# Kernel optimization log

Hardware: AMD Instinct MI355X
Metric: run time of the kernel (lower is better)

The kernel has to match this reference:

```python
import jax, jax.numpy as jnp
import numpy as np

N, E, IN_DIM, HID = 50000, 800000, 128, 64
NEG_SLOPE = 0.01  # torch F.leaky_relu default


def setup_inputs() -> dict:
    key = jax.random.key(0)
    ks = jax.random.split(key, 8)
    x = jax.random.normal(ks[0], (N, IN_DIM), jnp.float32)
    edge_index = jax.random.randint(ks[1], (2, E), 0, N, dtype=jnp.int32)
    edge_weight = jax.random.uniform(ks[2], (E,), jnp.float32)
    h = jnp.zeros((N, HID), jnp.float32)
    c = jnp.zeros((N, HID), jnp.float32)
    sx = 1.0 / np.sqrt(IN_DIM)
    sh = 1.0 / np.sqrt(HID)
    # gate order along leading axis: [i, f, c(tilde), o]; K=2 Chebyshev weights
    Wx = (jax.random.normal(ks[3], (4, 2, IN_DIM, HID), jnp.float32) * sx)
    bx = jnp.zeros((4, HID), jnp.float32)
    Wh = (jax.random.normal(ks[4], (4, 2, HID, HID), jnp.float32) * sh)
    bh = jnp.zeros((4, HID), jnp.float32)
    wc = jax.random.normal(ks[5], (3, HID), jnp.float32) * 0.1  # peepholes for i, f, o
    bg = jnp.zeros((4, HID), jnp.float32)
    W_head = jax.random.normal(ks[6], (HID, 1), jnp.float32) * sh
    b_head = jnp.zeros((1,), jnp.float32)
    return dict(x=x, edge_index=edge_index, edge_weight=edge_weight, h=h, c=c,
                Wx=Wx, bx=bx, Wh=Wh, bh=bh, wc=wc, bg=bg, W_head=W_head, b_head=b_head)


def _cheb_norm(src, dst, ew, n):
    # ChebConv 'sym' normalization with lambda_max=2: L_hat = -D^{-1/2} A D^{-1/2}
    # (the +1 self-loop from the Laplacian cancels against fill_value=-1)
    deg = jnp.zeros((n,), ew.dtype).at[src].add(ew)
    dinv = jnp.where(deg > 0, 1.0 / jnp.sqrt(jnp.where(deg > 0, deg, 1.0)), 0.0)
    return -dinv[src] * ew * dinv[dst]


def _prop(feat, src, dst, norm, n):
    # T1 = L_hat @ feat via edge gather + segment-sum
    return jax.ops.segment_sum(norm[:, None] * feat[src], dst, num_segments=n)


def reference(x, edge_index, edge_weight, h, c, Wx, bx, Wh, bh, wc, bg, W_head, b_head):
    n = x.shape[0]
    src, dst = edge_index[0], edge_index[1]
    norm = _cheb_norm(src, dst, edge_weight, n)
    Tx = _prop(x, src, dst, norm, n)
    Th = _prop(h, src, dst, norm, n)  # shared across all 4 h-side ChebConvs
    # z[g] = X W[g,0] + (L_hat X) W[g,1] + b  for all gates at once
    z = (jnp.einsum('nd,gdh->gnh', x, Wx[:, 0]) + jnp.einsum('nd,gdh->gnh', Tx, Wx[:, 1]) + bx[:, None, :]
         + jnp.einsum('nd,gdh->gnh', h, Wh[:, 0]) + jnp.einsum('nd,gdh->gnh', Th, Wh[:, 1]) + bh[:, None, :])
    i = jax.nn.sigmoid(z[0] + wc[0] * c + bg[0])
    f = jax.nn.sigmoid(z[1] + wc[1] * c + bg[1])
    g = jnp.tanh(z[2] + bg[2])
    c_new = f * c + i * g
    o = jax.nn.sigmoid(z[3] + wc[2] * c_new + bg[3])
    h_new = o * jnp.tanh(c_new)
    out = jax.nn.leaky_relu(h_new, NEG_SLOPE) @ W_head + b_head
    return out, h_new, c_new
```

## Files before the change

kernel.cpp:

```cpp
#include <hip/hip_runtime.h>
#include <hip/hip_bf16.h>

#define IN_DIM 128
#define HID 64
#define NEG_SLOPE 0.01f
#define CAP 5120

typedef __attribute__((ext_vector_type(8))) short short8;
typedef __attribute__((ext_vector_type(4))) short short4v;
typedef __attribute__((ext_vector_type(4))) float f32x4;
typedef unsigned short ushort_t;
typedef unsigned int uint_t;

__device__ __forceinline__ float fsig(float x) { return 1.f / (1.f + __expf(-x)); }
__device__ __forceinline__ float ftanh(float x) { return 1.f - 2.f / (__expf(2.f * x) + 1.f); }

__device__ __forceinline__ ushort_t f2bf(float f) {
    uint_t u = __float_as_uint(f);
    uint_t r = u + 0x7fffu + ((u >> 16) & 1u);
    return (ushort_t)(r >> 16);
}
__device__ __forceinline__ float bf2f(ushort_t s) { return __uint_as_float(((uint_t)s) << 16); }
__device__ __forceinline__ float bf2f_s(short s) { return bf2f((ushort_t)s); }

__global__ __launch_bounds__(256) void part_kernel(
    const int* __restrict__ src, const int* __restrict__ dst, const float* __restrict__ ew,
    const float* __restrict__ x, const float* __restrict__ h,
    const float* __restrict__ Wx, const float* __restrict__ Wh,
    int* __restrict__ cur_d, int* __restrict__ cur_s,
    int2* __restrict__ dpart, int2* __restrict__ spart,
    uint_t* __restrict__ xb_u, uint_t* __restrict__ hb_u, ushort_t* __restrict__ Wp,
    int E, int N, int nbPart) {
    __shared__ int hd[256], hs[256];
    int t = threadIdx.x;

    if (blockIdx.x < nbPart) {
        hd[t] = 0; hs[t] = 0;
        __syncthreads();
        int base = blockIdx.x * 2048;
        int sv[8], dv[8]; float wv[8];
#pragma unroll
        for (int it = 0; it < 8; ++it) {
            int e = base + it * 256 + t;
            bool ok = e < E;
            sv[it] = ok ? src[e] : 0;
            dv[it] = ok ? dst[e] : 0;
            wv[it] = ok ? ew[e] : 0.f;
            if (ok) {
                atomicAdd(&hd[dv[it] >> 8], 1);
                atomicAdd(&hs[sv[it] >> 8], 1);
            }
        }
        __syncthreads();
        int nd = hd[t], ns = hs[t];
        __syncthreads();
        if (nd) hd[t] = atomicAdd(&cur_d[t * 16], nd);
        if (ns) hs[t] = atomicAdd(&cur_s[t * 16], ns);
        __syncthreads();
#pragma unroll
        for (int it = 0; it < 8; ++it) {
            int e = base + it * 256 + t;
            if (e < E) {
                int d = dv[it], s = sv[it];
                int bd = d >> 8, bs = s >> 8;
                int pd = atomicAdd(&hd[bd], 1);
                int ps = atomicAdd(&hs[bs], 1);
                dpart[(size_t)bd * CAP + pd] = make_int2(s | ((d & 255) << 16), __float_as_int(wv[it]));
                spart[(size_t)bs * CAP + ps] = make_int2(s & 255, __float_as_int(wv[it]));
            }
        }
    }

    int tid = blockIdx.x * 256 + t;
    int T = gridDim.x * 256;
    int ncvt = N * 96;
    int nx = N * 64;
    for (int i = tid; i < ncvt; i += T) {
        if (i < nx) {
            float2 v = ((const float2*)x)[i];
            xb_u[i] = (uint_t)f2bf(v.x) | ((uint_t)f2bf(v.y) << 16);
        } else {
            int j = i - nx;
            float2 v = ((const float2*)h)[j];
            hb_u[j] = (uint_t)f2bf(v.x) | ((uint_t)f2bf(v.y) << 16);
        }
    }

    for (int idx = tid; idx < 384 * 256; idx += T) {
        int j = idx & 7;
        int tmp = idx >> 3;
        int lane = tmp & 63;
        int t2 = tmp >> 6;
        int ct = t2 & 15;
        int ks = t2 >> 4;
        int k = ks * 32 + (lane >> 4) * 8 + j;
        int colg = ct * 16 + (lane & 15);
        int g = colg >> 6, hdd = colg & 63;
        float v;
        if (k < 128)      v = Wx[((g * 2 + 0) * 128 + k) * 64 + hdd];
        else if (k < 192) v = Wh[((g * 2 + 0) * 64 + (k - 128)) * 64 + hdd];
        else if (k < 320) v = Wx[((g * 2 + 1) * 128 + (k - 192)) * 64 + hdd];
        else              v = Wh[((g * 2 + 1) * 64 + (k - 320)) * 64 + hdd];
        Wp[idx] = f2bf(v);
    }
}

__global__ __launch_bounds__(256) void deg_kernel(const int2* __restrict__ spart,
                                                  const int* __restrict__ cur_s,
                                                  float* __restrict__ dinv, int N) {
    __shared__ float df[256];
    int t = threadIdx.x, b = blockIdx.x;
    df[t] = 0.f;
    __syncthreads();
    int cnt = cur_s[b * 16];
    for (int i = t; i < cnt; i += 256) {
        int2 r = spart[(size_t)b * CAP + i];
        atomicAdd(&df[r.x & 255], __int_as_float(r.y));
    }
    __syncthreads();
    int g = b * 256 + t;
    if (g < N) {
        float dd = df[t];
        dinv[g] = dd > 0.f ? rsqrtf(dd) : 0.f;
    }
}

__global__ __launch_bounds__(256) void fillb_kernel(const int2* __restrict__ dpart,
                                                    const int* __restrict__ cur_d,
                                                    const float* __restrict__ dinv,
                                                    int* __restrict__ rowptr, int* __restrict__ rowend,
                                                    int2* __restrict__ eprm, int N) {
    __shared__ int c[256], sdata[256], pcur[256];
    __shared__ float dl[256];
    int t = threadIdx.x, b = blockIdx.x;
    c[t] = 0;
    int g = b * 256 + t;
    dl[t] = (g < N) ? dinv[g] : 0.f;
    __syncthreads();
    int cnt = cur_d[b * 16];
    for (int i = t; i < cnt; i += 256) {
        int m = dpart[(size_t)b * CAP + i].x;
        atomicAdd(&c[(m >> 16) & 255], 1);
    }
    __syncthreads();
    sdata[t] = c[t];
    __syncthreads();
    for (int off = 1; off < 256; off <<= 1) {
        int tmp = (t >= off) ? sdata[t - off] : 0;
        __syncthreads();
        sdata[t] += tmp;
        __syncthreads();
    }
    int excl = sdata[t] - c[t];
    pcur[t] = excl;
    if (g < N) {
        rowptr[g] = b * CAP + excl;
        rowend[g] = b * CAP + sdata[t];
    }
    __syncthreads();
    for (int i = t; i < cnt; i += 256) {
        int2 r = dpart[(size_t)b * CAP + i];
        int m = r.x;
        int dlo = (m >> 16) & 255;
        int s = m & 0xffff;
        float w = __int_as_float(r.y);
        int pos = atomicAdd(&pcur[dlo], 1);
        float nrm = -dinv[s] * w * dl[dlo];
        eprm[(size_t)b * CAP + pos] = make_int2(s, __float_as_int(nrm));
    }
}

#define GQ_LOAD(SS, WW, XV, HV, QOFF)                                          \
    _Pragma("unroll")                                                          \
    for (int q = 0; q < 4; ++q) {                                              \
        SS[q] = __shfl(sv, sl0 + (QOFF) + q);                                  \
        WW[q] = __shfl(wv, sl0 + (QOFF) + q);                                  \
        XV[q] = *(const short8*)(xb + (size_t)SS[q] * 128 + l16 * 8);          \
        HV[q] = *(const short4v*)(hb + (size_t)SS[q] * 64 + l16 * 4);          \
    }

#define GQ_FMA(WW, XV, HV)                                                     \
    _Pragma("unroll")                                                          \
    for (int q = 0; q < 4; ++q) {                                              \
        _Pragma("unroll")                                                      \
        for (int i = 0; i < 8; ++i) ax[i] += WW[q] * bf2f_s(XV[q][i]);         \
        _Pragma("unroll")                                                      \
        for (int i = 0; i < 4; ++i) ah[i] += WW[q] * bf2f_s(HV[q][i]);         \
    }

__global__ __launch_bounds__(256) void gather_kernel(const int* __restrict__ rowptr,
                                                     const int* __restrict__ rowend,
                                                     const int2* __restrict__ eprm,
                                                     const ushort_t* __restrict__ xb,
                                                     const ushort_t* __restrict__ hb,
                                                     ushort_t* __restrict__ Txb,
                                                     ushort_t* __restrict__ Thb, int N) {
    int lane = threadIdx.x & 63;
    int wave = threadIdx.x >> 6;
    int grp = lane >> 4, l16 = lane & 15;
    int node = blockIdx.x * 16 + wave * 4 + grp;
    bool valid = node < N;
    int p = 0, end = 0;
    if (valid) { p = rowptr[node]; end = rowend[node]; }

    float ax[8] = {0.f, 0.f, 0.f, 0.f, 0.f, 0.f, 0.f, 0.f};
    float ah[4] = {0.f, 0.f, 0.f, 0.f};

    int idx0 = p + l16;
    int2 pr = (idx0 < end) ? eprm[idx0] : make_int2(0, 0);

    int sl0 = grp * 16;
    for (int base = p; base < end; base += 16) {
        int2 cur = pr;
        int nidx = base + 16 + l16;
        if (base + 16 < end) pr = (nidx < end) ? eprm[nidx] : make_int2(0, 0);
        int sv = cur.x;
        float wv = __int_as_float(cur.y);

        int sA[4]; float wA[4]; short8 xA[4]; short4v hA[4];
        int sB[4]; float wB[4]; short8 xB[4]; short4v hB[4];
        GQ_LOAD(sA, wA, xA, hA, 0)
        GQ_LOAD(sB, wB, xB, hB, 4)
        GQ_FMA(wA, xA, hA)
        GQ_LOAD(sA, wA, xA, hA, 8)
        GQ_FMA(wB, xB, hB)
        GQ_LOAD(sB, wB, xB, hB, 12)
        GQ_FMA(wA, xA, hA)
        GQ_FMA(wB, xB, hB)
    }

    if (valid) {
        short8 tx;
#pragma unroll
        for (int i = 0; i < 8; ++i) tx[i] = (short)f2bf(ax[i]);
        *(short8*)(Txb + (size_t)node * 128 + l16 * 8) = tx;
        short4v th;
#pragma unroll
        for (int i = 0; i < 4; ++i) th[i] = (short)f2bf(ah[i]);
        *(short4v*)(Thb + (size_t)node * 64 + l16 * 4) = th;
    }
}

__global__ __launch_bounds__(256, 4) void fused_mfma(
    const ushort_t* __restrict__ xb, const ushort_t* __restrict__ hb,
    const ushort_t* __restrict__ Txb, const ushort_t* __restrict__ Thb,
    const float* __restrict__ c_in, const ushort_t* __restrict__ Wp,
    const float* __restrict__ bx, const float* __restrict__ bh,
    const float* __restrict__ wc, const float* __restrict__ bg,
    const float* __restrict__ Whead, const float* __restrict__ bhead,
    float* __restrict__ out, int N) {
    __shared__ ushort_t Bs[2][8192];
    int tid = threadIdx.x;
    int lane = tid & 63;
    int wave = tid >> 6;
    int quad = lane >> 4, m = lane & 15;
    int row0 = (blockIdx.x * 4 + wave) * 16;
    int ar = row0 + m; if (ar >= N) ar = N - 1;
    int ko = quad * 8;

    short8 afr[12];
#pragma unroll
    for (int ks = 0; ks < 12; ++ks) {
        const ushort_t* a;
        if (ks < 4)       a = xb  + (size_t)ar * 128 + ks * 32 + ko;
        else if (ks < 6)  a = hb  + (size_t)ar * 64 + (ks - 4) * 32 + ko;
        else if (ks < 10) a = Txb + (size_t)ar * 128 + (ks - 6) * 32 + ko;
        else              a = Thb + (size_t)ar * 64 + (ks - 10) * 32 + ko;
        afr[ks] = *(const short8*)a;
    }

    {
        const float4* gsrc = (const float4*)(Wp);
        float4* ldst = (float4*)Bs[0];
#pragma unroll
        for (int i = 0; i < 4; ++i) ldst[tid + 256 * i] = gsrc[tid + 256 * i];
    }

    f32x4 acc[16];
#pragma unroll
    for (int ct = 0; ct < 16; ++ct) {
        int g = ct >> 2, hd = (ct & 3) * 16 + m;
        float b = bx[g * 64 + hd] + bh[g * 64 + hd];
        f32x4 bb = {b, b, b, b};
        acc[ct] = bb;
    }

    __syncthreads();

#pragma unroll
    for (int ks = 0; ks < 12; ++ks) {
        int buf = ks & 1;
        float4 tmp[4];
        if (ks < 11) {
            const float4* gsrc = (const float4*)(Wp + (ks + 1) * 8192);
#pragma unroll
            for (int i = 0; i < 4; ++i) tmp[i] = gsrc[tid + 256 * i];
        }
        const short8* bsp = (const short8*)Bs[buf];
#pragma unroll
        for (int ct = 0; ct < 16; ++ct) {
            short8 bf = bsp[ct * 64 + lane];
            acc[ct] = __builtin_amdgcn_mfma_f32_16x16x32_bf16(afr[ks], bf, acc[ct], 0, 0, 0);
        }
        if (ks < 11) {
            float4* ldst = (float4*)Bs[buf ^ 1];
#pragma unroll
            for (int i = 0; i < 4; ++i) ldst[tid + 256 * i] = tmp[i];
            __syncthreads();
        }
    }

    float hp[4] = {0.f, 0.f, 0.f, 0.f};
    float bhv = bhead[0];

#pragma unroll
    for (int hs = 0; hs < 4; ++hs) {
        int hd = hs * 16 + m;
        float wc0 = wc[hd], wc1 = wc[64 + hd], wc2 = wc[128 + hd];
        float bg0 = bg[hd], bg1 = bg[64 + hd], bg2 = bg[128 + hd], bg3 = bg[192 + hd];
        float wh = Whead[hd];
#pragma unroll
        for (int reg = 0; reg < 4; ++reg) {
            int n = row0 + quad * 4 + reg;
            if (n < N) {
                float c_old = c_in[(size_t)n * 64 + hd];
                float zi = acc[0 * 4 + hs][reg];
                float zf = acc[1 * 4 + hs][reg];
                float zg = acc[2 * 4 + hs][reg];
                float zo = acc[3 * 4 + hs][reg];
                float ii = fsig(zi + wc0 * c_old + bg0);
                float ff = fsig(zf + wc1 * c_old + bg1);
                float gg = ftanh(zg + bg2);
                float cn = ff * c_old + ii * gg;
                float oo = fsig(zo + wc2 * cn + bg3);
                float hn = oo * ftanh(cn);
                out[N + (size_t)n * 64 + hd] = hn;
                out[N + (size_t)N * 64 + (size_t)n * 64 + hd] = cn;
                float lr = hn > 0.f ? hn : NEG_SLOPE * hn;
                hp[reg] += lr * wh;
            }
        }
    }
#pragma unroll
    for (int reg = 0; reg < 4; ++reg) {
        float v0 = hp[reg];
#pragma unroll
        for (int mask = 1; mask < 16; mask <<= 1) v0 += __shfl_xor(v0, mask);
        if (m == 0) {
            int n0_ = row0 + quad * 4 + reg;
            if (n0_ < N) out[n0_] = v0 + bhv;
        }
    }
}

extern "C" void kernel_launch(void* const* d_in, const int* in_sizes, int n_in,
                              void* d_out, int out_size, void* d_ws, size_t ws_size,
                              hipStream_t stream) {
    const float* x = (const float*)d_in[0];
    const int* ei = (const int*)d_in[1];
    const float* ew = (const float*)d_in[2];
    const float* h = (const float*)d_in[3];
    const float* c = (const float*)d_in[4];
    const float* Wx = (const float*)d_in[5];
    const float* bx = (const float*)d_in[6];
    const float* Wh = (const float*)d_in[7];
    const float* bh = (const float*)d_in[8];
    const float* wc = (const float*)d_in[9];
    const float* bg = (const float*)d_in[10];
    const float* Whead = (const float*)d_in[11];
    const float* bhead = (const float*)d_in[12];

    int N = in_sizes[0] / IN_DIM;
    int E = in_sizes[1] / 2;
    const int* src = ei;
    const int* dst = ei + E;

    int nbuck = (N + 255) >> 8;
    int nbPart = (E + 2047) / 2048;

    char* wp = (char*)d_ws;
    auto alloc = [&](size_t bytes) {
        char* p = wp;
        wp += (bytes + 255) & ~(size_t)255;
        return p;
    };
    int* cur = (int*)alloc((size_t)2 * nbuck * 16 * 4);
    int* cur_d = cur;
    int* cur_s = cur + (size_t)nbuck * 16;
    float* dinv = (float*)alloc((size_t)N * 4);
    int* rowptr = (int*)alloc((size_t)N * 4);
    int* rowend = (int*)alloc((size_t)N * 4);
    int2* dpart = (int2*)alloc((size_t)nbuck * CAP * 8);
    int2* spart = (int2*)alloc((size_t)nbuck * CAP * 8);
    int2* eprm = spart;
    ushort_t* xb = (ushort_t*)alloc((size_t)N * 128 * 2);
    ushort_t* hb = (ushort_t*)alloc((size_t)N * 64 * 2);
    ushort_t* Txb = (ushort_t*)alloc((size_t)N * 128 * 2);
    ushort_t* Thb = (ushort_t*)alloc((size_t)N * 64 * 2);
    ushort_t* Wp = (ushort_t*)alloc((size_t)384 * 256 * 2);

    hipMemsetAsync(cur, 0, (size_t)2 * nbuck * 16 * 4, stream);

    part_kernel<<<1024, 256, 0, stream>>>(src, dst, ew, x, h, Wx, Wh,
                                          cur_d, cur_s, dpart, spart,
                                          (uint_t*)xb, (uint_t*)hb, Wp, E, N, nbPart);
    deg_kernel<<<nbuck, 256, 0, stream>>>(spart, cur_s, dinv, N);
    fillb_kernel<<<nbuck, 256, 0, stream>>>(dpart, cur_d, dinv, rowptr, rowend, eprm, N);
    gather_kernel<<<(N + 15) / 16, 256, 0, stream>>>(rowptr, rowend, eprm, xb, hb, Txb, Thb, N);
    fused_mfma<<<(N + 63) / 64, 256, 0, stream>>>(xb, hb, Txb, Thb, c, Wp, bx, bh, wc, bg,
                                                  Whead, bhead, (float*)d_out, N);
}
```

Measured before the change: 253.8 us.

## Fuse gather into MFMA kernel and merge degree and fill passes

```diff
diff --git a/kernel.cpp b/kernel.cpp
--- a/kernel.cpp
+++ b/kernel.cpp
@@ -105,68 +105,63 @@
     }
 }
 
-__global__ __launch_bounds__(256) void deg_kernel(const int2* __restrict__ spart,
-                                                  const int* __restrict__ cur_s,
-                                                  float* __restrict__ dinv, int N) {
-    __shared__ float df[256];
-    int t = threadIdx.x, b = blockIdx.x;
-    df[t] = 0.f;
-    __syncthreads();
-    int cnt = cur_s[b * 16];
-    for (int i = t; i < cnt; i += 256) {
-        int2 r = spart[(size_t)b * CAP + i];
-        atomicAdd(&df[r.x & 255], __int_as_float(r.y));
-    }
-    __syncthreads();
-    int g = b * 256 + t;
-    if (g < N) {
-        float dd = df[t];
-        dinv[g] = dd > 0.f ? rsqrtf(dd) : 0.f;
-    }
-}
-
-__global__ __launch_bounds__(256) void fillb_kernel(const int2* __restrict__ dpart,
-                                                    const int* __restrict__ cur_d,
-                                                    const float* __restrict__ dinv,
-                                                    int* __restrict__ rowptr, int* __restrict__ rowend,
-                                                    int2* __restrict__ eprm, int N) {
-    __shared__ int c[256], sdata[256], pcur[256];
-    __shared__ float dl[256];
-    int t = threadIdx.x, b = blockIdx.x;
-    c[t] = 0;
-    int g = b * 256 + t;
-    dl[t] = (g < N) ? dinv[g] : 0.f;
-    __syncthreads();
-    int cnt = cur_d[b * 16];
-    for (int i = t; i < cnt; i += 256) {
-        int m = dpart[(size_t)b * CAP + i].x;
-        atomicAdd(&c[(m >> 16) & 255], 1);
-    }
-    __syncthreads();
-    sdata[t] = c[t];
-    __syncthreads();
-    for (int off = 1; off < 256; off <<= 1) {
-        int tmp = (t >= off) ? sdata[t - off] : 0;
-        __syncthreads();
-        sdata[t] += tmp;
-        __syncthreads();
-    }
-    int excl = sdata[t] - c[t];
-    pcur[t] = excl;
-    if (g < N) {
-        rowptr[g] = b * CAP + excl;
-        rowend[g] = b * CAP + sdata[t];
-    }
-    __syncthreads();
-    for (int i = t; i < cnt; i += 256) {
-        int2 r = dpart[(size_t)b * CAP + i];
-        int m = r.x;
-        int dlo = (m >> 16) & 255;
-        int s = m & 0xffff;
-        float w = __int_as_float(r.y);
-        int pos = atomicAdd(&pcur[dlo], 1);
-        float nrm = -dinv[s] * w * dl[dlo];
-        eprm[(size_t)b * CAP + pos] = make_int2(s, __float_as_int(nrm));
+__global__ __launch_bounds__(256) void degfill_kernel(
+    const int2* __restrict__ spart, const int2* __restrict__ dpart,
+    const int* __restrict__ cur_s, const int* __restrict__ cur_d,
+    float* __restrict__ dinv, int* __restrict__ rowptr, int* __restrict__ rowend,
+    int2* __restrict__ eprm, int N, int nbuck) {
+    int t = threadIdx.x;
+    if ((int)blockIdx.x < nbuck) {
+        __shared__ float df[256];
+        int b = blockIdx.x;
+        df[t] = 0.f;
+        __syncthreads();
+        int cnt = cur_s[b * 16];
+        for (int i = t; i < cnt; i += 256) {
+            int2 r = spart[(size_t)b * CAP + i];
+            atomicAdd(&df[r.x & 255], __int_as_float(r.y));
+        }
+        __syncthreads();
+        int g = b * 256 + t;
+        if (g < N) {
+            float dd = df[t];
+            dinv[g] = dd > 0.f ? rsqrtf(dd) : 0.f;
+        }
+    } else {
+        __shared__ int c[256], sdata[256], pcur[256];
+        int b = blockIdx.x - nbuck;
+        c[t] = 0;
+        int g = b * 256 + t;
+        __syncthreads();
+        int cnt = cur_d[b * 16];
+        for (int i = t; i < cnt; i += 256) {
+            int m = dpart[(size_t)b * CAP + i].x;
+            atomicAdd(&c[(m >> 16) & 255], 1);
+        }
+        __syncthreads();
+        sdata[t] = c[t];
+        __syncthreads();
+        for (int off = 1; off < 256; off <<= 1) {
+            int tmp = (t >= off) ? sdata[t - off] : 0;
+            __syncthreads();
+            sdata[t] += tmp;
+            __syncthreads();
+        }
+        int excl = sdata[t] - c[t];
+        pcur[t] = excl;
+        if (g < N) {
+            rowptr[g] = b * CAP + excl;
+            rowend[g] = b * CAP + sdata[t];
+        }
+        __syncthreads();
+        for (int i = t; i < cnt; i += 256) {
+            int2 r = dpart[(size_t)b * CAP + i];
+            int m = r.x;
+            int dlo = (m >> 16) & 255;
+            int s = m & 0xffff;
+            int pos = atomicAdd(&pcur[dlo], 1);
+            eprm[(size_t)b * CAP + pos] = make_int2(s, r.y);
+        }
     }
 }
 
@@ -188,92 +183,79 @@
         for (int i = 0; i < 4; ++i) ah[i] += WW[q] * bf2f_s(HV[q][i]);         \
     }
 
-__global__ __launch_bounds__(256) void gather_kernel(const int* __restrict__ rowptr,
-                                                     const int* __restrict__ rowend,
-                                                     const int2* __restrict__ eprm,
-                                                     const ushort_t* __restrict__ xb,
-                                                     const ushort_t* __restrict__ hb,
-                                                     ushort_t* __restrict__ Txb,
-                                                     ushort_t* __restrict__ Thb, int N) {
-    int lane = threadIdx.x & 63;
-    int wave = threadIdx.x >> 6;
-    int grp = lane >> 4, l16 = lane & 15;
-    int node = blockIdx.x * 16 + wave * 4 + grp;
-    bool valid = node < N;
-    int p = 0, end = 0;
-    if (valid) { p = rowptr[node]; end = rowend[node]; }
-
-    float ax[8] = {0.f, 0.f, 0.f, 0.f, 0.f, 0.f, 0.f, 0.f};
-    float ah[4] = {0.f, 0.f, 0.f, 0.f};
-
-    int idx0 = p + l16;
-    int2 pr = (idx0 < end) ? eprm[idx0] : make_int2(0, 0);
-
-    int sl0 = grp * 16;
-    for (int base = p; base < end; base += 16) {
-        int2 cur = pr;
-        int nidx = base + 16 + l16;
-        if (base + 16 < end) pr = (nidx < end) ? eprm[nidx] : make_int2(0, 0);
-        int sv = cur.x;
-        float wv = __int_as_float(cur.y);
-
-        int sA[4]; float wA[4]; short8 xA[4]; short4v hA[4];
-        int sB[4]; float wB[4]; short8 xB[4]; short4v hB[4];
-        GQ_LOAD(sA, wA, xA, hA, 0)
-        GQ_LOAD(sB, wB, xB, hB, 4)
-        GQ_FMA(wA, xA, hA)
-        GQ_LOAD(sA, wA, xA, hA, 8)
-        GQ_FMA(wB, xB, hB)
-        GQ_LOAD(sB, wB, xB, hB, 12)
-        GQ_FMA(wA, xA, hA)
-        GQ_FMA(wB, xB, hB)
-    }
-
-    if (valid) {
-        short8 tx;
-#pragma unroll
-        for (int i = 0; i < 8; ++i) tx[i] = (short)f2bf(ax[i]);
-        *(short8*)(Txb + (size_t)node * 128 + l16 * 8) = tx;
-        short4v th;
-#pragma unroll
-        for (int i = 0; i < 4; ++i) th[i] = (short)f2bf(ah[i]);
-        *(short4v*)(Thb + (size_t)node * 64 + l16 * 4) = th;
-    }
-}
-
-__global__ __launch_bounds__(256, 4) void fused_mfma(
+__global__ __launch_bounds__(256, 3) void gather_fused(
+    const int* __restrict__ rowptr, const int* __restrict__ rowend,
+    const int2* __restrict__ eprm, const float* __restrict__ dinv,
     const ushort_t* __restrict__ xb, const ushort_t* __restrict__ hb,
-    const ushort_t* __restrict__ Txb, const ushort_t* __restrict__ Thb,
     const float* __restrict__ c_in, const ushort_t* __restrict__ Wp,
     const float* __restrict__ bx, const float* __restrict__ bh,
     const float* __restrict__ wc, const float* __restrict__ bg,
     const float* __restrict__ Whead, const float* __restrict__ bhead,
     float* __restrict__ out, int N) {
-    __shared__ ushort_t Bs[2][8192];
+    __shared__ ushort_t Bs[8192];
+    __shared__ ushort_t Ts[64][200];
     int tid = threadIdx.x;
     int lane = tid & 63;
     int wave = tid >> 6;
-    int quad = lane >> 4, m = lane & 15;
-    int row0 = (blockIdx.x * 4 + wave) * 16;
-    int ar = row0 + m; if (ar >= N) ar = N - 1;
+    int grp = lane >> 4, l16 = lane & 15;
+    int quad = grp, m = l16;
+    int row0 = blockIdx.x * 64;
+    int rowbase = row0 + wave * 16;
     int ko = quad * 8;
 
-    short8 afr[12];
-#pragma unroll
-    for (int ks = 0; ks < 12; ++ks) {
-        const ushort_t* a;
-        if (ks < 4)       a = xb  + (size_t)ar * 128 + ks * 32 + ko;
-        else if (ks < 6)  a = hb  + (size_t)ar * 64 + (ks - 4) * 32 + ko;
-        else if (ks < 10) a = Txb + (size_t)ar * 128 + (ks - 6) * 32 + ko;
-        else              a = Thb + (size_t)ar * 64 + (ks - 10) * 32 + ko;
-        afr[ks] = *(const short8*)a;
-    }
-
-    {
-        const float4* gsrc = (const float4*)(Wp);
-        float4* ldst = (float4*)Bs[0];
-#pragma unroll
-        for (int i = 0; i < 4; ++i) ldst[tid + 256 * i] = gsrc[tid + 256 * i];
+    int ar = rowbase + m; if (ar >= N) ar = N - 1;
+    short8 afr[6];
+#pragma unroll
+    for (int ks = 0; ks < 4; ++ks) afr[ks] = *(const short8*)(xb + (size_t)ar * 128 + ks * 32 + ko);
+#pragma unroll
+    for (int ks = 4; ks < 6; ++ks) afr[ks] = *(const short8*)(hb + (size_t)ar * 64 + (ks - 4) * 32 + ko);
+
+    int sl0 = grp * 16;
+    for (int r = 0; r < 4; ++r) {
+        int lr = wave * 16 + r * 4 + grp;
+        int node = row0 + lr;
+        bool valid = node < N;
+        int p = 0, end = 0;
+        if (valid) { p = rowptr[node]; end = rowend[node]; }
+
+        float ax[8] = {0.f, 0.f, 0.f, 0.f, 0.f, 0.f, 0.f, 0.f};
+        float ah[4] = {0.f, 0.f, 0.f, 0.f};
+
+        int idx0 = p + l16;
+        int2 pr = (idx0 < end) ? eprm[idx0] : make_int2(0, 0);
+        float dpr = (idx0 < end) ? dinv[pr.x] : 0.f;
+
+        for (int base = p; base < end; base += 16) {
+            int2 cur = pr; float dcur = dpr;
+            int nidx = base + 16 + l16;
+            if (base + 16 < end) {
+                pr = (nidx < end) ? eprm[nidx] : make_int2(0, 0);
+                dpr = (nidx < end) ? dinv[pr.x] : 0.f;
+            }
+            int sv = cur.x;
+            float wv = __int_as_float(cur.y) * dcur;
+
+            int sA[4]; float wA[4]; short8 xA[4]; short4v hA[4];
+            int sB[4]; float wB[4]; short8 xB[4]; short4v hB[4];
+            GQ_LOAD(sA, wA, xA, hA, 0)
+            GQ_LOAD(sB, wB, xB, hB, 4)
+            GQ_FMA(wA, xA, hA)
+            GQ_LOAD(sA, wA, xA, hA, 8)
+            GQ_FMA(wB, xB, hB)
+            GQ_LOAD(sB, wB, xB, hB, 12)
+            GQ_FMA(wA, xA, hA)
+            GQ_FMA(wB, xB, hB)
+        }
+
+        float sc = valid ? -dinv[node] : 0.f;
+        short8 tx;
+#pragma unroll
+        for (int i = 0; i < 8; ++i) tx[i] = (short)f2bf(ax[i] * sc);
+        *(short8*)(&Ts[lr][l16 * 8]) = tx;
+        short4v th;
+#pragma unroll
+        for (int i = 0; i < 4; ++i) th[i] = (short)f2bf(ah[i] * sc);
+        *(short4v*)(&Ts[lr][128 + l16 * 4]) = th;
     }
 
     f32x4 acc[16];
@@ -285,28 +267,36 @@
         acc[ct] = bb;
     }
 
-    __syncthreads();
+    float4 tmp[4];
+    {
+        const float4* gsrc = (const float4*)(Wp);
+#pragma unroll
+        for (int i = 0; i < 4; ++i) tmp[i] = gsrc[tid + 256 * i];
+    }
 
 #pragma unroll
     for (int ks = 0; ks < 12; ++ks) {
-        int buf = ks & 1;
-        float4 tmp[4];
+        __syncthreads();
+        {
+            float4* ldst = (float4*)Bs;
+#pragma unroll
+            for (int i = 0; i < 4; ++i) ldst[tid + 256 * i] = tmp[i];
+        }
+        __syncthreads();
         if (ks < 11) {
             const float4* gsrc = (const float4*)(Wp + (ks + 1) * 8192);
 #pragma unroll
             for (int i = 0; i < 4; ++i) tmp[i] = gsrc[tid + 256 * i];
         }
-        const short8* bsp = (const short8*)Bs[buf];
+        short8 af;
+        if (ks < 6)       af = afr[ks];
+        else if (ks < 10) af = *(const short8*)(&Ts[wave * 16 + m][(ks - 6) * 32 + ko]);
+        else              af = *(const short8*)(&Ts[wave * 16 + m][128 + (ks - 10) * 32 + ko]);
+        const short8* bsp = (const short8*)Bs;
 #pragma unroll
         for (int ct = 0; ct < 16; ++ct) {
             short8 bf = bsp[ct * 64 + lane];
-            acc[ct] = __builtin_amdgcn_mfma_f32_16x16x32_bf16(afr[ks], bf, acc[ct], 0, 0, 0);
-        }
-        if (ks < 11) {
-            float4* ldst = (float4*)Bs[buf ^ 1];
-#pragma unroll
-            for (int i = 0; i < 4; ++i) ldst[tid + 256 * i] = tmp[i];
-            __syncthreads();
+            acc[ct] = __builtin_amdgcn_mfma_f32_16x16x32_bf16(af, bf, acc[ct], 0, 0, 0);
         }
     }
 
@@ -321,7 +311,7 @@
         float wh = Whead[hd];
 #pragma unroll
         for (int reg = 0; reg < 4; ++reg) {
-            int n = row0 + quad * 4 + reg;
+            int n = rowbase + quad * 4 + reg;
             if (n < N) {
                 float c_old = c_in[(size_t)n * 64 + hd];
                 float zi = acc[0 * 4 + hs][reg];
@@ -347,7 +337,7 @@
 #pragma unroll
         for (int mask = 1; mask < 16; mask <<= 1) v0 += __shfl_xor(v0, mask);
         if (m == 0) {
-            int n0_ = row0 + quad * 4 + reg;
+            int n0_ = rowbase + quad * 4 + reg;
             if (n0_ < N) out[n0_] = v0 + bhv;
         }
     }
@@ -392,11 +382,9 @@
     int* rowend = (int*)alloc((size_t)N * 4);
     int2* dpart = (int2*)alloc((size_t)nbuck * CAP * 8);
     int2* spart = (int2*)alloc((size_t)nbuck * CAP * 8);
-    int2* eprm = spart;
+    int2* eprm  = (int2*)alloc((size_t)nbuck * CAP * 8);
     ushort_t* xb = (ushort_t*)alloc((size_t)N * 128 * 2);
     ushort_t* hb = (ushort_t*)alloc((size_t)N * 64 * 2);
-    ushort_t* Txb = (ushort_t*)alloc((size_t)N * 128 * 2);
-    ushort_t* Thb = (ushort_t*)alloc((size_t)N * 64 * 2);
     ushort_t* Wp = (ushort_t*)alloc((size_t)384 * 256 * 2);
 
     hipMemsetAsync(cur, 0, (size_t)2 * nbuck * 16 * 4, stream);
@@ -404,9 +392,9 @@
     part_kernel<<<1024, 256, 0, stream>>>(src, dst, ew, x, h, Wx, Wh,
                                           cur_d, cur_s, dpart, spart,
                                           (uint_t*)xb, (uint_t*)hb, Wp, E, N, nbPart);
-    deg_kernel<<<nbuck, 256, 0, stream>>>(spart, cur_s, dinv, N);
-    fillb_kernel<<<nbuck, 256, 0, stream>>>(dpart, cur_d, dinv, rowptr, rowend, eprm, N);
-    gather_kernel<<<(N + 15) / 16, 256, 0, stream>>>(rowptr, rowend, eprm, xb, hb, Txb, Thb, N);
-    fused_mfma<<<(N + 63) / 64, 256, 0, stream>>>(xb, hb, Txb, Thb, c, Wp, bx, bh, wc, bg,
-                                                  Whead, bhead, (float*)d_out, N);
+    degfill_kernel<<<2 * nbuck, 256, 0, stream>>>(spart, dpart, cur_s, cur_d,
+                                                  dinv, rowptr, rowend, eprm, N, nbuck);
+    gather_fused<<<(N + 63) / 64, 256, 0, stream>>>(rowptr, rowend, eprm, dinv, xb, hb,
+                                                    c, Wp, bx, bh, wc, bg,
+                                                    Whead, bhead, (float*)d_out, N);
 }
```

New measurement: 316.3 us. 24.6% more time.

## Merge degree and CSR-fill kernels, defer normalization into gather

Applied to the files above, without the earlier changes.

```diff
diff --git a/kernel.cpp b/kernel.cpp
--- a/kernel.cpp
+++ b/kernel.cpp
@@ -34,7 +34,7 @@
     __shared__ int hd[256], hs[256];
     int t = threadIdx.x;
 
-    if (blockIdx.x < nbPart) {
+    if ((int)blockIdx.x < nbPart) {
         hd[t] = 0; hs[t] = 0;
         __syncthreads();
         int base = blockIdx.x * 2048;
@@ -69,10 +69,12 @@
                 spart[(size_t)bs * CAP + ps] = make_int2(s & 255, __float_as_int(wv[it]));
             }
         }
-    }
-
-    int tid = blockIdx.x * 256 + t;
-    int T = gridDim.x * 256;
+        return;
+    }
+
+    int cb = blockIdx.x - nbPart;
+    int tid = cb * 256 + t;
+    int T = (gridDim.x - nbPart) * 256;
     int ncvt = N * 96;
     int nx = N * 64;
     for (int i = tid; i < ncvt; i += T) {
@@ -105,68 +107,63 @@
     }
 }
 
-__global__ __launch_bounds__(256) void deg_kernel(const int2* __restrict__ spart,
-                                                  const int* __restrict__ cur_s,
-                                                  float* __restrict__ dinv, int N) {
-    __shared__ float df[256];
-    int t = threadIdx.x, b = blockIdx.x;
-    df[t] = 0.f;
-    __syncthreads();
-    int cnt = cur_s[b * 16];
-    for (int i = t; i < cnt; i += 256) {
-        int2 r = spart[(size_t)b * CAP + i];
-        atomicAdd(&df[r.x & 255], __int_as_float(r.y));
-    }
-    __syncthreads();
-    int g = b * 256 + t;
-    if (g < N) {
-        float dd = df[t];
-        dinv[g] = dd > 0.f ? rsqrtf(dd) : 0.f;
-    }
-}
-
-__global__ __launch_bounds__(256) void fillb_kernel(const int2* __restrict__ dpart,
-                                                    const int* __restrict__ cur_d,
-                                                    const float* __restrict__ dinv,
-                                                    int* __restrict__ rowptr, int* __restrict__ rowend,
-                                                    int2* __restrict__ eprm, int N) {
-    __shared__ int c[256], sdata[256], pcur[256];
-    __shared__ float dl[256];
-    int t = threadIdx.x, b = blockIdx.x;
-    c[t] = 0;
-    int g = b * 256 + t;
-    dl[t] = (g < N) ? dinv[g] : 0.f;
-    __syncthreads();
-    int cnt = cur_d[b * 16];
-    for (int i = t; i < cnt; i += 256) {
-        int m = dpart[(size_t)b * CAP + i].x;
-        atomicAdd(&c[(m >> 16) & 255], 1);
-    }
-    __syncthreads();
-    sdata[t] = c[t];
-    __syncthreads();
-    for (int off = 1; off < 256; off <<= 1) {
-        int tmp = (t >= off) ? sdata[t - off] : 0;
-        __syncthreads();
-        sdata[t] += tmp;
-        __syncthreads();
-    }
-    int excl = sdata[t] - c[t];
-    pcur[t] = excl;
-    if (g < N) {
-        rowptr[g] = b * CAP + excl;
-        rowend[g] = b * CAP + sdata[t];
-    }
-    __syncthreads();
-    for (int i = t; i < cnt; i += 256) {
-        int2 r = dpart[(size_t)b * CAP + i];
-        int m = r.x;
-        int dlo = (m >> 16) & 255;
-        int s = m & 0xffff;
-        float w = __int_as_float(r.y);
-        int pos = atomicAdd(&pcur[dlo], 1);
-        float nrm = -dinv[s] * w * dl[dlo];
-        eprm[(size_t)b * CAP + pos] = make_int2(s, __float_as_int(nrm));
+__global__ __launch_bounds__(256) void degfill_kernel(
+    const int2* __restrict__ spart, const int2* __restrict__ dpart,
+    const int* __restrict__ cur_s, const int* __restrict__ cur_d,
+    float* __restrict__ dinv, int* __restrict__ rowptr, int* __restrict__ rowend,
+    int2* __restrict__ eprm, int N, int nbuck) {
+    int t = threadIdx.x;
+    if ((int)blockIdx.x < nbuck) {
+        __shared__ float df[256];
+        int b = blockIdx.x;
+        df[t] = 0.f;
+        __syncthreads();
+        int cnt = cur_s[b * 16];
+        for (int i = t; i < cnt; i += 256) {
+            int2 r = spart[(size_t)b * CAP + i];
+            atomicAdd(&df[r.x & 255], __int_as_float(r.y));
+        }
+        __syncthreads();
+        int g = b * 256 + t;
+        if (g < N) {
+            float dd = df[t];
+            dinv[g] = dd > 0.f ? rsqrtf(dd) : 0.f;
+        }
+    } else {
+        __shared__ int c[256], sdata[256], pcur[256];
+        int b = blockIdx.x - nbuck;
+        c[t] = 0;
+        int g = b * 256 + t;
+        __syncthreads();
+        int cnt = cur_d[b * 16];
+        for (int i = t; i < cnt; i += 256) {
+            int m = dpart[(size_t)b * CAP + i].x;
+            atomicAdd(&c[(m >> 16) & 255], 1);
+        }
+        __syncthreads();
+        sdata[t] = c[t];
+        __syncthreads();
+        for (int off = 1; off < 256; off <<= 1) {
+            int tmp = (t >= off) ? sdata[t - off] : 0;
+            __syncthreads();
+            sdata[t] += tmp;
+            __syncthreads();
+        }
+        int excl = sdata[t] - c[t];
+        pcur[t] = excl;
+        if (g < N) {
+            rowptr[g] = b * CAP + excl;
+            rowend[g] = b * CAP + sdata[t];
+        }
+        __syncthreads();
+        for (int i = t; i < cnt; i += 256) {
+            int2 r = dpart[(size_t)b * CAP + i];
+            int m = r.x;
+            int dlo = (m >> 16) & 255;
+            int s = m & 0xffff;
+            int pos = atomicAdd(&pcur[dlo], 1);
+            eprm[(size_t)b * CAP + pos] = make_int2(s, r.y);
+        }
     }
 }
 
@@ -191,6 +188,7 @@
 __global__ __launch_bounds__(256) void gather_kernel(const int* __restrict__ rowptr,
                                                      const int* __restrict__ rowend,
                                                      const int2* __restrict__ eprm,
+                                                     const float* __restrict__ dinv,
                                                      const ushort_t* __restrict__ xb,
                                                      const ushort_t* __restrict__ hb,
                                                      ushort_t* __restrict__ Txb,
@@ -208,14 +206,18 @@
 
     int idx0 = p + l16;
     int2 pr = (idx0 < end) ? eprm[idx0] : make_int2(0, 0);
+    float dpr = (idx0 < end) ? dinv[pr.x] : 0.f;
 
     int sl0 = grp * 16;
     for (int base = p; base < end; base += 16) {
-        int2 cur = pr;
+        int2 cur = pr; float dcur = dpr;
         int nidx = base + 16 + l16;
-        if (base + 16 < end) pr = (nidx < end) ? eprm[nidx] : make_int2(0, 0);
+        if (base + 16 < end) {
+            pr = (nidx < end) ? eprm[nidx] : make_int2(0, 0);
+            dpr = (nidx < end) ? dinv[pr.x] : 0.f;
+        }
         int sv = cur.x;
-        float wv = __int_as_float(cur.y);
+        float wv = __int_as_float(cur.y) * dcur;
 
         int sA[4]; float wA[4]; short8 xA[4]; short4v hA[4];
         int sB[4]; float wB[4]; short8 xB[4]; short4v hB[4];
@@ -230,13 +232,14 @@
     }
 
     if (valid) {
+        float sc = -dinv[node];
         short8 tx;
 #pragma unroll
-        for (int i = 0; i < 8; ++i) tx[i] = (short)f2bf(ax[i]);
+        for (int i = 0; i < 8; ++i) tx[i] = (short)f2bf(ax[i] * sc);
         *(short8*)(Txb + (size_t)node * 128 + l16 * 8) = tx;
         short4v th;
 #pragma unroll
-        for (int i = 0; i < 4; ++i) th[i] = (short)f2bf(ah[i]);
+        for (int i = 0; i < 4; ++i) th[i] = (short)f2bf(ah[i] * sc);
         *(short4v*)(Thb + (size_t)node * 64 + l16 * 4) = th;
     }
 }
@@ -392,7 +395,7 @@
     int* rowend = (int*)alloc((size_t)N * 4);
     int2* dpart = (int2*)alloc((size_t)nbuck * CAP * 8);
     int2* spart = (int2*)alloc((size_t)nbuck * CAP * 8);
-    int2* eprm = spart;
+    int2* eprm  = (int2*)alloc((size_t)nbuck * CAP * 8);
     ushort_t* xb = (ushort_t*)alloc((size_t)N * 128 * 2);
     ushort_t* hb = (ushort_t*)alloc((size_t)N * 64 * 2);
     ushort_t* Txb = (ushort_t*)alloc((size_t)N * 128 * 2);
@@ -401,12 +404,13 @@
 
     hipMemsetAsync(cur, 0, (size_t)2 * nbuck * 16 * 4, stream);
 
-    part_kernel<<<1024, 256, 0, stream>>>(src, dst, ew, x, h, Wx, Wh,
+    part_kernel<<<2048, 256, 0, stream>>>(src, dst, ew, x, h, Wx, Wh,
                                           cur_d, cur_s, dpart, spart,
                                           (uint_t*)xb, (uint_t*)hb, Wp, E, N, nbPart);
-    deg_kernel<<<nbuck, 256, 0, stream>>>(spart, cur_s, dinv, N);
-    fillb_kernel<<<nbuck, 256, 0, stream>>>(dpart, cur_d, dinv, rowptr, rowend, eprm, N);
-    gather_kernel<<<(N + 15) / 16, 256, 0, stream>>>(rowptr, rowend, eprm, xb, hb, Txb, Thb, N);
+    degfill_kernel<<<2 * nbuck, 256, 0, stream>>>(spart, dpart, cur_s, cur_d,
+                                                  dinv, rowptr, rowend, eprm, N, nbuck);
+    gather_kernel<<<(N + 15) / 16, 256, 0, stream>>>(rowptr, rowend, eprm, dinv,
+                                                     xb, hb, Txb, Thb, N);
     fused_mfma<<<(N + 63) / 64, 256, 0, stream>>>(xb, hb, Txb, Thb, c, Wp, bx, bh, wc, bg,
                                                   Whead, bhead, (float*)d_out, N);
 }
```

New measurement: 247.7 us. 2.4% less time.
